# Kernel tuning notes

Hardware: AMD Instinct MI355X
Metric: run time of the kernel (lower is better)

## Reference

```python
import jax, jax.numpy as jnp
import numpy as np

HEADS = 16
ROPE_BASE = 10000.0


def _rope(x):
    # x: [b, h, n, d]. lucidrains partial rotary: RotaryEmbedding(head_dim//2)
    # rotates only the first rot_dim = d//2 channels, interleaved-pair style.
    d = x.shape[-1]
    rot = d // 2
    inv_freq = 1.0 / (ROPE_BASE ** (jnp.arange(0, rot, 2, dtype=jnp.float32) / rot))  # [rot//2]
    pos = jnp.arange(x.shape[2], dtype=jnp.float32)
    freqs = pos[:, None] * inv_freq[None, :]                  # [n, rot//2]
    cos, sin = jnp.cos(freqs), jnp.sin(freqs)
    xr, xp = x[..., :rot], x[..., rot:]
    x1, x2 = xr[..., 0::2], xr[..., 1::2]                     # interleaved pairs
    o1 = x1 * cos - x2 * sin
    o2 = x2 * cos + x1 * sin
    xr_out = jnp.stack([o1, o2], axis=-1).reshape(xr.shape)   # re-interleave
    return jnp.concatenate([xr_out, xp], axis=-1)


def setup_inputs() -> dict:
    key = jax.random.key(0)
    k0, k1 = jax.random.split(key)
    B, N, D = 2, 2048, 2048
    x = jax.random.normal(k0, (B, N, D), dtype=jnp.float32)
    W_qkv = jax.random.normal(k1, (3 * D, D), dtype=jnp.float32) * (D ** -0.5)
    b_qkv = jnp.zeros((3 * D,), dtype=jnp.float32)
    return {"x": x, "W_qkv": W_qkv, "b_qkv": b_qkv}


def reference(x, W_qkv, b_qkv):
    B, N, D = x.shape
    H = HEADS
    hd = D // H
    qkv = x @ W_qkv.T + b_qkv                                  # [b, n, 3d]
    q, k, v = jnp.split(qkv, 3, axis=-1)
    to_heads = lambda t: t.reshape(B, N, H, hd).transpose(0, 2, 1, 3)  # b h n d
    q, k, v = to_heads(q), to_heads(k), to_heads(v)
    q, k = _rope(q), _rope(k)
    scale = 1.0 / np.sqrt(hd)
    scores = jnp.einsum('bhnd,bhmd->bhnm', q, k) * scale
    causal = jnp.tril(jnp.ones((N, N), dtype=bool))
    scores = jnp.where(causal, scores, -jnp.inf)
    attn = jax.nn.softmax(scores, axis=-1)
    y = jnp.einsum('bhnm,bhmd->bhnd', attn, v)
    return y.transpose(0, 2, 1, 3).reshape(B, N, D)
```

## Files before the change

### kernel.cpp

```cpp
#include <hip/hip_runtime.h>
#include <hip/hip_bf16.h>
#include <math.h>

typedef unsigned short u16;
typedef unsigned int u32;
typedef __attribute__((ext_vector_type(8))) short bf16x8;
typedef __attribute__((ext_vector_type(4))) float f32x4;

#define B_ 2
#define N_ 2048
#define D_ 2048
#define H_ 16
#define HD 128
#define GK 2048

__device__ __forceinline__ u16 f2bf(float f) {
  u32 u = __float_as_uint(f);
  u = (u + 0x7fffu + ((u >> 16) & 1u)) >> 16;
  return (u16)u;
}

__device__ __forceinline__ u32 cvtpk(float lo, float hi) {
  u32 r;
  asm("v_cvt_pk_bf16_f32 %0, %1, %2" : "=v"(r) : "v"(lo), "v"(hi));
  return r;
}

__device__ __forceinline__ void gload_lds16(const void* g, void* l) {
  __builtin_amdgcn_global_load_lds(
      (const __attribute__((address_space(1))) u32*)g,
      (__attribute__((address_space(3))) u32*)l, 16, 0, 0);
}

__global__ __launch_bounds__(256) void prep_kernel(
    const float* __restrict__ x, const float* __restrict__ Wq,
    u16* __restrict__ Xb, u16* __restrict__ Wb, float* __restrict__ tbl) {
  const int i0 = blockIdx.x * blockDim.x + threadIdx.x;
  const int st = gridDim.x * blockDim.x;
  const int n4x = (B_ * N_ * D_) / 4;
  const int n4w = (3 * D_ * D_) / 4;
  for (int i = i0; i < n4x + n4w; i += st) {
    float4 v;
    ushort4 o;
    if (i < n4x) {
      v = ((const float4*)x)[i];
      o.x = f2bf(v.x); o.y = f2bf(v.y); o.z = f2bf(v.z); o.w = f2bf(v.w);
      ((ushort4*)Xb)[i] = o;
    } else {
      v = ((const float4*)Wq)[i - n4x];
      o.x = f2bf(v.x); o.y = f2bf(v.y); o.z = f2bf(v.z); o.w = f2bf(v.w);
      ((ushort4*)Wb)[i - n4x] = o;
    }
  }
  for (int i = i0; i < N_ * 32; i += st) {
    int pos = i >> 5, p = i & 31;
    double inv = pow(10000.0, -(double)p / 32.0);
    double a = (double)pos * inv;
    tbl[2 * i]     = (float)cos(a);
    tbl[2 * i + 1] = (float)sin(a);
  }
}

__global__ __launch_bounds__(512, 2) void qkv_gemm_kernel(
    const u16* __restrict__ X, const u16* __restrict__ W,
    const float* __restrict__ bias, const float* __restrict__ tbl,
    u16* __restrict__ Qo, u16* __restrict__ Ko, u16* __restrict__ Vo) {
  __shared__ char smem[147456];
  const int tid = threadIdx.x;
  const int lane = tid & 63;
  const int w = tid >> 6;
  const int wm = w >> 2, wn = w & 3;
  const int l15 = lane & 15, l4 = lane >> 4;

  const int bid = blockIdx.x;
  const int wg = (bid & 7) * 64 + (bid >> 3);
  const int n0 = (wg & 31) * 192;
  const int m0 = (wg >> 5) * 256;

  const int aof0 = (l4 * 16) ^ ((l15 & 7) << 4);
  const int aof1 = (64 + l4 * 16) ^ ((l15 & 7) << 4);
  const int kfA = wm ? aof1 : aof0;
  const int ksA = wm ? aof0 : aof1;

  int srowA[2], scolA[2];
#pragma unroll
  for (int p = 0; p < 2; ++p) {
    int o = (w * 2 + p) * 1024 + lane * 16;
    int lo = o ^ (((o >> 7) & 7) << 4);
    srowA[p] = lo >> 7;
    scolA[p] = (lo & 127) >> 1;
  }
  const int oB = w * 1024 + lane * 16;
  const int loB = oB ^ (((oB >> 7) & 7) << 4);
  const int srowB = loB >> 7, scolB = (loB & 127) >> 1;

  f32x4 acc[8][3];
#pragma unroll
  for (int fm = 0; fm < 8; ++fm)
#pragma unroll
    for (int fn = 0; fn < 3; ++fn)
#pragma unroll
      for (int q = 0; q < 4; ++q) acc[fm][fn][q] = 0.f;

  auto stageA = [&](char* Abase, int half, int k0) {
#pragma unroll
    for (int p = 0; p < 2; ++p) {
      gload_lds16(X + (size_t)(m0 + half * 128 + srowA[p]) * GK + k0 + scolA[p],
                  Abase + half * 16384 + (w * 2 + p) * 1024);
    }
  };
  auto stageB = [&](char* Bbase, int chunk, int k0) {
    gload_lds16(W + (size_t)(n0 + chunk * 64 + srowB) * GK + k0 + scolB,
                Bbase + chunk * 8192 + w * 1024);
  };

  const int NK = GK / 64;

  stageA(smem, 0, 0); stageA(smem, 1, 0);
  stageB(smem + 98304, 0, 0); stageB(smem + 98304, 1, 0); stageB(smem + 98304, 2, 0);
  stageA(smem + 32768, 0, 64); stageA(smem + 32768, 1, 64);
  asm volatile("s_waitcnt vmcnt(4)" ::: "memory");
  __builtin_amdgcn_s_barrier();

  int at = 0;
  for (int T = 0; T < NK; ++T) {
    const int bt = T & 1;
    int an2 = at + 2; if (an2 >= 3) an2 -= 3;
    const char* Ab = smem + at * 32768 + wm * 16384;
    const char* Bb = smem + 98304 + bt * 24576;
    char* Bn = smem + 98304 + (bt ^ 1) * 24576;
    char* An = smem + an2 * 32768;
    const int kn1 = (T + 1) * 64, kn2 = (T + 2) * 64;
    const bool hasB = (T + 1 < NK), hasA = (T + 2 < NK);

    bf16x8 bf_[3], bs_[3], aq[4];

#pragma unroll
    for (int fn = 0; fn < 3; ++fn)
      bf_[fn] = *(const bf16x8*)(Bb + (wn * 48 + fn * 16 + l15) * 128 + kfA);
#pragma unroll
    for (int fm = 0; fm < 4; ++fm)
      aq[fm] = *(const bf16x8*)(Ab + (fm * 16 + l15) * 128 + kfA);
    if (hasB) { stageB(Bn, 0, kn1); stageB(Bn, 1, kn1); stageB(Bn, 2, kn1); }
    __builtin_amdgcn_s_setprio(1);
#pragma unroll
    for (int fm = 0; fm < 4; ++fm)
#pragma unroll
      for (int fn = 0; fn < 3; ++fn)
        acc[fm][fn] = __builtin_amdgcn_mfma_f32_16x16x32_bf16(aq[fm], bf_[fn], acc[fm][fn], 0, 0, 0);
    __builtin_amdgcn_s_setprio(0);

#pragma unroll
    for (int fm = 0; fm < 4; ++fm)
      aq[fm] = *(const bf16x8*)(Ab + ((fm + 4) * 16 + l15) * 128 + kfA);
    __builtin_amdgcn_s_setprio(1);
#pragma unroll
    for (int fm = 0; fm < 4; ++fm)
#pragma unroll
      for (int fn = 0; fn < 3; ++fn)
        acc[fm + 4][fn] = __builtin_amdgcn_mfma_f32_16x16x32_bf16(aq[fm], bf_[fn], acc[fm + 4][fn], 0, 0, 0);
    __builtin_amdgcn_s_setprio(0);

#pragma unroll
    for (int fn = 0; fn < 3; ++fn)
      bs_[fn] = *(const bf16x8*)(Bb + (wn * 48 + fn * 16 + l15) * 128 + ksA);
#pragma unroll
    for (int fm = 0; fm < 4; ++fm)
      aq[fm] = *(const bf16x8*)(Ab + (fm * 16 + l15) * 128 + ksA);
    if (hasA) { stageA(An, 0, kn2); stageA(An, 1, kn2); }
    __builtin_amdgcn_s_setprio(1);
#pragma unroll
    for (int fm = 0; fm < 4; ++fm)
#pragma unroll
      for (int fn = 0; fn < 3; ++fn)
        acc[fm][fn] = __builtin_amdgcn_mfma_f32_16x16x32_bf16(aq[fm], bs_[fn], acc[fm][fn], 0, 0, 0);
    __builtin_amdgcn_s_setprio(0);

#pragma unroll
    for (int fm = 0; fm < 4; ++fm)
      aq[fm] = *(const bf16x8*)(Ab + ((fm + 4) * 16 + l15) * 128 + ksA);
    if (hasA) {
      asm volatile("s_waitcnt vmcnt(4)" ::: "memory");
    } else {
      asm volatile("s_waitcnt vmcnt(0)" ::: "memory");
    }
    __builtin_amdgcn_s_setprio(1);
#pragma unroll
    for (int fm = 0; fm < 4; ++fm)
#pragma unroll
      for (int fn = 0; fn < 3; ++fn)
        acc[fm + 4][fn] = __builtin_amdgcn_mfma_f32_16x16x32_bf16(aq[fm], bs_[fn], acc[fm + 4][fn], 0, 0, 0);
    __builtin_amdgcn_s_setprio(0);
    __builtin_amdgcn_s_barrier();

    at = (at + 1 == 3) ? 0 : at + 1;
  }

  const float QSCALE = 0.08838834764831845f;
#pragma unroll
  for (int fn = 0; fn < 3; ++fn) {
    int gn = n0 + wn * 48 + fn * 16 + l15;
    float bv = bias[gn];
    int sec = gn >> 11;
    int wi = gn & 2047;
    int h = wi >> 7;
    int d = wi & 127;
    u16* dstbase = (sec == 0) ? Qo : (sec == 1) ? Ko : Vo;
    float mulf = (sec == 0) ? QSCALE : 1.f;
    bool doRope = (sec < 2) && (d < 64);
    int pidx = d >> 1;
    bool odd = (d & 1) != 0;
#pragma unroll
    for (int fm = 0; fm < 8; ++fm) {
#pragma unroll
      for (int j = 0; j < 4; ++j) {
        int gm = m0 + wm * 128 + fm * 16 + l4 * 4 + j;
        int bb = gm >> 11;
        int pos = gm & 2047;
        float v = acc[fm][fn][j] + bv;
        float pr = __shfl_xor(v, 1);
        float ov = v;
        if (doRope) {
          float2 cs = ((const float2*)tbl)[pos * 32 + pidx];
          ov = odd ? (v * cs.x + pr * cs.y) : (v * cs.x - pr * cs.y);
        }
        dstbase[(size_t)((bb * H_ + h) * N_ + pos) * HD + d] = f2bf(ov * mulf);
      }
    }
  }
}

__global__ __launch_bounds__(256, 2) void flash_kernel(
    const u16* __restrict__ Q, const u16* __restrict__ K, const u16* __restrict__ V,
    float* __restrict__ Out) {
  __shared__ char smem[51200];

  const int tid = threadIdx.x, lane = tid & 63, w = tid >> 6;
  const int l15 = lane & 15, l4 = lane >> 4;

  const int bid = blockIdx.x;
  const int xcd = bid & 7, s_ = bid >> 3;
  const int bh = xcd * 4 + (s_ & 3);
  const int x = 31 - (s_ >> 2);
  const int bb = bh >> 4, h = bh & 15;
  const size_t base = (size_t)bh * (N_ * HD);
  const int q0 = x * 64;
  const int nt = x + 1;

  bf16x8 qf[4];
  {
    const u16* qp = Q + base + (size_t)(q0 + w * 16 + l15) * HD + l4 * 8;
#pragma unroll
    for (int kf = 0; kf < 4; ++kf) qf[kf] = *(const bf16x8*)(qp + kf * 32);
  }

  float m_r = -1e30f, l_r = 0.f;
  f32x4 accO[8];
#pragma unroll
  for (int df = 0; df < 8; ++df)
#pragma unroll
    for (int q = 0; q < 4; ++q) accO[df][q] = 0.f;

  auto stageK = [&](int buf, int t0) {
    const u16* kb = K + base + (size_t)t0 * HD;
    char* kt = smem + buf * 16384;
#pragma unroll
    for (int i = 0; i < 4; ++i) {
      int c = w * 4 + i;
      int o = c * 1024 + lane * 16;
      int lo = o ^ (((o >> 8) & 7) << 4);
      gload_lds16(kb + (lo >> 1), kt + c * 1024);
    }
  };
  auto loadV = [&](int t0, bf16x8* vr) {
    const u16* vp = V + base + (size_t)(t0 + lane) * HD + w * 32;
#pragma unroll
    for (int i = 0; i < 4; ++i) vr[i] = *(const bf16x8*)(vp + i * 8);
  };
  auto writeV = [&](const bf16x8* vr) {
    u16* vt = (u16*)(smem + 32768);
#pragma unroll
    for (int i = 0; i < 4; ++i)
#pragma unroll
      for (int jj = 0; jj < 8; ++jj)
        vt[(w * 32 + i * 8 + jj) * 72 + lane] = (u16)vr[i][jj];
  };

  const int src0 = l15 + 32 * (l4 & 1);
  const int src1 = src0 + 16;
  const int half = l4 >> 1;
  union U8 { u32 u[4]; bf16x8 v; };

  bf16x8 vreg[4];
  stageK(0, 0);
  loadV(0, vreg);
  __syncthreads();
  writeV(vreg);
  __syncthreads();

  for (int t = 0; t < nt; ++t) {
    const int cur = t & 1;
    const int t0 = t * 64;
    const bool pre = (t + 1 < nt);
    if (pre) { stageK(cur ^ 1, t0 + 64); loadV(t0 + 64, vreg); }

    const char* kt = smem + cur * 16384;
    const u16* vt = (const u16*)(smem + 32768);

    f32x4 s[4];
#pragma unroll
    for (int cf = 0; cf < 4; ++cf) {
#pragma unroll
      for (int q = 0; q < 4; ++q) s[cf][q] = 0.f;
      int row = cf * 16 + l15;
      int sw = (row & 7) << 4;
#pragma unroll
      for (int kf = 0; kf < 4; ++kf) {
        int off = (row * 256 + kf * 64 + l4 * 16) ^ sw;
        bf16x8 kfrag = *(const bf16x8*)(kt + off);
        s[cf] = __builtin_amdgcn_mfma_f32_16x16x32_bf16(kfrag, qf[kf], s[cf], 0, 0, 0);
      }
    }

    const int qbase = q0 + w * 16;
    if (t0 + 63 > qbase) {
      const int qg = qbase + l15;
#pragma unroll
      for (int cf = 0; cf < 4; ++cf)
#pragma unroll
        for (int j = 0; j < 4; ++j) {
          int kvg = t0 + cf * 16 + l4 * 4 + j;
          if (kvg > qg) s[cf][j] = -1e30f;
        }
    }

    float pmax = s[0][0];
#pragma unroll
    for (int cf = 0; cf < 4; ++cf)
#pragma unroll
      for (int j = 0; j < 4; ++j) pmax = fmaxf(pmax, s[cf][j]);
    pmax = fmaxf(pmax, __shfl_xor(pmax, 16));
    pmax = fmaxf(pmax, __shfl_xor(pmax, 32));

    if (!__all(pmax <= m_r + 8.f)) {
      float mn = fmaxf(m_r, pmax);
      float rs = __expf(m_r - mn);
      m_r = mn;
      l_r *= rs;
#pragma unroll
      for (int df = 0; df < 8; ++df)
#pragma unroll
        for (int j = 0; j < 4; ++j) accO[df][j] *= rs;
    }

    u32 pk[4][2];
    float ps = 0.f;
#pragma unroll
    for (int cf = 0; cf < 4; ++cf) {
      float p0 = __expf(s[cf][0] - m_r);
      float p1 = __expf(s[cf][1] - m_r);
      float p2 = __expf(s[cf][2] - m_r);
      float p3 = __expf(s[cf][3] - m_r);
      ps += (p0 + p1) + (p2 + p3);
      pk[cf][0] = cvtpk(p0, p1);
      pk[cf][1] = cvtpk(p2, p3);
    }
    ps += __shfl_xor(ps, 16);
    ps += __shfl_xor(ps, 32);
    l_r += ps;

#pragma unroll
    for (int c = 0; c < 2; ++c) {
      const int c2 = 2 * c;
      u32 a0 = (u32)__shfl((int)pk[c2][0], src0);
      u32 b0 = (u32)__shfl((int)pk[c2 + 1][0], src0);
      u32 a1 = (u32)__shfl((int)pk[c2][1], src0);
      u32 b1 = (u32)__shfl((int)pk[c2 + 1][1], src0);
      u32 a2 = (u32)__shfl((int)pk[c2][0], src1);
      u32 b2 = (u32)__shfl((int)pk[c2 + 1][0], src1);
      u32 a3 = (u32)__shfl((int)pk[c2][1], src1);
      u32 b3 = (u32)__shfl((int)pk[c2 + 1][1], src1);
      U8 pu;
      pu.u[0] = half ? b0 : a0;
      pu.u[1] = half ? b1 : a1;
      pu.u[2] = half ? b2 : a2;
      pu.u[3] = half ? b3 : a3;
#pragma unroll
      for (int df = 0; df < 8; ++df) {
        bf16x8 vf = *(const bf16x8*)(vt + (df * 16 + l15) * 72 + c * 32 + l4 * 8);
        accO[df] = __builtin_amdgcn_mfma_f32_16x16x32_bf16(vf, pu.v, accO[df], 0, 0, 0);
      }
    }

    __syncthreads();
    if (pre) writeV(vreg);
    __syncthreads();
  }

  float* Obuf = (float*)(smem + w * 8448);
  const int l31 = lane & 31;
  {
    float inv = 1.f / l_r;
#pragma unroll
    for (int df = 0; df < 8; ++df) {
      f32x4 v = accO[df];
#pragma unroll
      for (int j = 0; j < 4; ++j) v[j] *= inv;
      *(f32x4*)&Obuf[l15 * 132 + df * 16 + l4 * 4] = v;
    }
  }
#pragma unroll
  for (int p = 0; p < 8; ++p) {
    int row = p * 2 + (lane >> 5);
    f32x4 v = *(const f32x4*)&Obuf[row * 132 + l31 * 4];
    int qg = q0 + w * 16 + row;
    *(f32x4*)&Out[(size_t)(bb * N_ + qg) * D_ + h * HD + l31 * 4] = v;
  }
}

extern "C" void kernel_launch(void* const* d_in, const int* in_sizes, int n_in,
                              void* d_out, int out_size, void* d_ws, size_t ws_size,
                              hipStream_t stream) {
  const float* x  = (const float*)d_in[0];
  const float* Wq = (const float*)d_in[1];
  const float* bq = (const float*)d_in[2];
  float* out = (float*)d_out;
  char* ws = (char*)d_ws;

  u16* Qb  = (u16*)(ws);
  u16* Kb  = (u16*)(ws + 16777216);
  u16* Vb  = (u16*)(ws + 2 * 16777216);
  u16* Xb  = (u16*)(ws + 3 * 16777216);
  u16* Wb  = (u16*)(ws + 4 * 16777216);
  float* tbl = (float*)(ws + 4 * 16777216 + 25165824);

  prep_kernel<<<2048, 256, 0, stream>>>(x, Wq, Xb, Wb, tbl);
  qkv_gemm_kernel<<<512, 512, 0, stream>>>(Xb, Wb, bq, tbl, Qb, Kb, Vb);
  flash_kernel<<<1024, 256, 0, stream>>>(Qb, Kb, Vb, out);
}
```

Baseline: 232.4 us.

## Shrink QKV GEMM tile to 128x192 with 4 waves and double-buffered pipeline

The QKV projection GEMM moves from 512-thread blocks computing 256x192 tiles with triple-buffered A and staggered prefetch to 256-thread blocks computing 128x192 tiles with plain double buffering. Block count doubles to 1024 and the block-to-tile swizzle changes. Shared memory per block drops from 144KB to 80KB, which allows more blocks per CU and spreads the work more evenly across CUs. In exchange each block reuses its data less (more global/L2 traffic per FLOP), and the loop now waits for all outstanding loads (vmcnt(0)) each iteration, which shortens how far loads can run ahead of compute.

```diff
diff --git a/kernel.cpp b/kernel.cpp
--- a/kernel.cpp
+++ b/kernel.cpp
@@ -61,38 +61,32 @@
   }
 }
 
-__global__ __launch_bounds__(512, 2) void qkv_gemm_kernel(
+__global__ __launch_bounds__(256, 2) void qkv_gemm_kernel(
     const u16* __restrict__ X, const u16* __restrict__ W,
     const float* __restrict__ bias, const float* __restrict__ tbl,
     u16* __restrict__ Qo, u16* __restrict__ Ko, u16* __restrict__ Vo) {
-  __shared__ char smem[147456];
+  __shared__ char smem[81920];
   const int tid = threadIdx.x;
   const int lane = tid & 63;
   const int w = tid >> 6;
-  const int wm = w >> 2, wn = w & 3;
   const int l15 = lane & 15, l4 = lane >> 4;
 
   const int bid = blockIdx.x;
-  const int wg = (bid & 7) * 64 + (bid >> 3);
-  const int n0 = (wg & 31) * 192;
-  const int m0 = (wg >> 5) * 256;
+  const int i_ = bid >> 3;
+  const int m0 = (i_ >> 2) * 128;
+  const int n0 = ((bid & 7) * 4 + (i_ & 3)) * 192;
 
   const int aof0 = (l4 * 16) ^ ((l15 & 7) << 4);
   const int aof1 = (64 + l4 * 16) ^ ((l15 & 7) << 4);
-  const int kfA = wm ? aof1 : aof0;
-  const int ksA = wm ? aof0 : aof1;
-
-  int srowA[2], scolA[2];
-#pragma unroll
-  for (int p = 0; p < 2; ++p) {
-    int o = (w * 2 + p) * 1024 + lane * 16;
+
+  int soRow[6], soCol[6];
+#pragma unroll
+  for (int c = 0; c < 6; ++c) {
+    int o = c * 4096 + tid * 16;
     int lo = o ^ (((o >> 7) & 7) << 4);
-    srowA[p] = lo >> 7;
-    scolA[p] = (lo & 127) >> 1;
-  }
-  const int oB = w * 1024 + lane * 16;
-  const int loB = oB ^ (((oB >> 7) & 7) << 4);
-  const int srowB = loB >> 7, scolB = (loB & 127) >> 1;
+    soRow[c] = lo >> 7;
+    soCol[c] = (lo & 127) >> 1;
+  }
 
   f32x4 acc[8][3];
 #pragma unroll
@@ -102,104 +96,96 @@
 #pragma unroll
       for (int q = 0; q < 4; ++q) acc[fm][fn][q] = 0.f;
 
-  auto stageA = [&](char* Abase, int half, int k0) {
-#pragma unroll
-    for (int p = 0; p < 2; ++p) {
-      gload_lds16(X + (size_t)(m0 + half * 128 + srowA[p]) * GK + k0 + scolA[p],
-                  Abase + half * 16384 + (w * 2 + p) * 1024);
-    }
+  auto stageA = [&](char* Ab, int k0) {
+#pragma unroll
+    for (int c = 0; c < 4; ++c)
+      gload_lds16(X + (size_t)(m0 + soRow[c]) * GK + k0 + soCol[c],
+                  Ab + c * 4096 + tid * 16);
   };
-  auto stageB = [&](char* Bbase, int chunk, int k0) {
-    gload_lds16(W + (size_t)(n0 + chunk * 64 + srowB) * GK + k0 + scolB,
-                Bbase + chunk * 8192 + w * 1024);
+  auto stageB = [&](char* Bb, int k0) {
+#pragma unroll
+    for (int c = 0; c < 6; ++c)
+      gload_lds16(W + (size_t)(n0 + soRow[c]) * GK + k0 + soCol[c],
+                  Bb + c * 4096 + tid * 16);
   };
 
   const int NK = GK / 64;
 
-  stageA(smem, 0, 0); stageA(smem, 1, 0);
-  stageB(smem + 98304, 0, 0); stageB(smem + 98304, 1, 0); stageB(smem + 98304, 2, 0);
-  stageA(smem + 32768, 0, 64); stageA(smem + 32768, 1, 64);
-  asm volatile("s_waitcnt vmcnt(4)" ::: "memory");
+  stageA(smem, 0);
+  stageB(smem + 32768, 0);
+  asm volatile("s_waitcnt vmcnt(0)" ::: "memory");
   __builtin_amdgcn_s_barrier();
 
-  int at = 0;
   for (int T = 0; T < NK; ++T) {
-    const int bt = T & 1;
-    int an2 = at + 2; if (an2 >= 3) an2 -= 3;
-    const char* Ab = smem + at * 32768 + wm * 16384;
-    const char* Bb = smem + 98304 + bt * 24576;
-    char* Bn = smem + 98304 + (bt ^ 1) * 24576;
-    char* An = smem + an2 * 32768;
-    const int kn1 = (T + 1) * 64, kn2 = (T + 2) * 64;
-    const bool hasB = (T + 1 < NK), hasA = (T + 2 < NK);
-
-    bf16x8 bf_[3], bs_[3], aq[4];
+    const int cb = T & 1;
+    const char* Ab = smem + cb * 16384;
+    const char* Bb = smem + 32768 + cb * 24576;
+    char* An = smem + (cb ^ 1) * 16384;
+    char* Bn = smem + 32768 + (cb ^ 1) * 24576;
+    const int kn = (T + 1) * 64;
+    const bool nx = (T + 1 < NK);
+
+    bf16x8 bl[3], bh[3], aq[4];
 
 #pragma unroll
     for (int fn = 0; fn < 3; ++fn)
-      bf_[fn] = *(const bf16x8*)(Bb + (wn * 48 + fn * 16 + l15) * 128 + kfA);
-#pragma unroll
-    for (int fm = 0; fm < 4; ++fm)
-      aq[fm] = *(const bf16x8*)(Ab + (fm * 16 + l15) * 128 + kfA);
-    if (hasB) { stageB(Bn, 0, kn1); stageB(Bn, 1, kn1); stageB(Bn, 2, kn1); }
+      bl[fn] = *(const bf16x8*)(Bb + (w * 48 + fn * 16 + l15) * 128 + aof0);
+#pragma unroll
+    for (int fm = 0; fm < 4; ++fm)
+      aq[fm] = *(const bf16x8*)(Ab + (fm * 16 + l15) * 128 + aof0);
+    if (nx) stageB(Bn, kn);
     __builtin_amdgcn_s_setprio(1);
 #pragma unroll
     for (int fm = 0; fm < 4; ++fm)
 #pragma unroll
       for (int fn = 0; fn < 3; ++fn)
-        acc[fm][fn] = __builtin_amdgcn_mfma_f32_16x16x32_bf16(aq[fm], bf_[fn], acc[fm][fn], 0, 0, 0);
+        acc[fm][fn] = __builtin_amdgcn_mfma_f32_16x16x32_bf16(aq[fm], bl[fn], acc[fm][fn], 0, 0, 0);
     __builtin_amdgcn_s_setprio(0);
 
 #pragma unroll
     for (int fm = 0; fm < 4; ++fm)
-      aq[fm] = *(const bf16x8*)(Ab + ((fm + 4) * 16 + l15) * 128 + kfA);
+      aq[fm] = *(const bf16x8*)(Ab + ((fm + 4) * 16 + l15) * 128 + aof0);
     __builtin_amdgcn_s_setprio(1);
 #pragma unroll
     for (int fm = 0; fm < 4; ++fm)
 #pragma unroll
       for (int fn = 0; fn < 3; ++fn)
-        acc[fm + 4][fn] = __builtin_amdgcn_mfma_f32_16x16x32_bf16(aq[fm], bf_[fn], acc[fm + 4][fn], 0, 0, 0);
+        acc[fm + 4][fn] = __builtin_amdgcn_mfma_f32_16x16x32_bf16(aq[fm], bl[fn], acc[fm + 4][fn], 0, 0, 0);
     __builtin_amdgcn_s_setprio(0);
 
 #pragma unroll
     for (int fn = 0; fn < 3; ++fn)
-      bs_[fn] = *(const bf16x8*)(Bb + (wn * 48 + fn * 16 + l15) * 128 + ksA);
-#pragma unroll
-    for (int fm = 0; fm < 4; ++fm)
-      aq[fm] = *(const bf16x8*)(Ab + (fm * 16 + l15) * 128 + ksA);
-    if (hasA) { stageA(An, 0, kn2); stageA(An, 1, kn2); }
+      bh[fn] = *(const bf16x8*)(Bb + (w * 48 + fn * 16 + l15) * 128 + aof1);
+#pragma unroll
+    for (int fm = 0; fm < 4; ++fm)
+      aq[fm] = *(const bf16x8*)(Ab + (fm * 16 + l15) * 128 + aof1);
+    if (nx) stageA(An, kn);
     __builtin_amdgcn_s_setprio(1);
 #pragma unroll
     for (int fm = 0; fm < 4; ++fm)
 #pragma unroll
       for (int fn = 0; fn < 3; ++fn)
-        acc[fm][fn] = __builtin_amdgcn_mfma_f32_16x16x32_bf16(aq[fm], bs_[fn], acc[fm][fn], 0, 0, 0);
+        acc[fm][fn] = __builtin_amdgcn_mfma_f32_16x16x32_bf16(aq[fm], bh[fn], acc[fm][fn], 0, 0, 0);
     __builtin_amdgcn_s_setprio(0);
 
 #pragma unroll
     for (int fm = 0; fm < 4; ++fm)
-      aq[fm] = *(const bf16x8*)(Ab + ((fm + 4) * 16 + l15) * 128 + ksA);
-    if (hasA) {
-      asm volatile("s_waitcnt vmcnt(4)" ::: "memory");
-    } else {
-      asm volatile("s_waitcnt vmcnt(0)" ::: "memory");
-    }
+      aq[fm] = *(const bf16x8*)(Ab + ((fm + 4) * 16 + l15) * 128 + aof1);
+    asm volatile("s_waitcnt vmcnt(0)" ::: "memory");
     __builtin_amdgcn_s_setprio(1);
 #pragma unroll
     for (int fm = 0; fm < 4; ++fm)
 #pragma unroll
       for (int fn = 0; fn < 3; ++fn)
-        acc[fm + 4][fn] = __builtin_amdgcn_mfma_f32_16x16x32_bf16(aq[fm], bs_[fn], acc[fm + 4][fn], 0, 0, 0);
+        acc[fm + 4][fn] = __builtin_amdgcn_mfma_f32_16x16x32_bf16(aq[fm], bh[fn], acc[fm + 4][fn], 0, 0, 0);
     __builtin_amdgcn_s_setprio(0);
     __builtin_amdgcn_s_barrier();
-
-    at = (at + 1 == 3) ? 0 : at + 1;
   }
 
   const float QSCALE = 0.08838834764831845f;
 #pragma unroll
   for (int fn = 0; fn < 3; ++fn) {
-    int gn = n0 + wn * 48 + fn * 16 + l15;
+    int gn = n0 + w * 48 + fn * 16 + l15;
     float bv = bias[gn];
     int sec = gn >> 11;
     int wi = gn & 2047;
@@ -214,7 +200,7 @@
     for (int fm = 0; fm < 8; ++fm) {
 #pragma unroll
       for (int j = 0; j < 4; ++j) {
-        int gm = m0 + wm * 128 + fm * 16 + l4 * 4 + j;
+        int gm = m0 + fm * 16 + l4 * 4 + j;
         int bb = gm >> 11;
         int pos = gm & 2047;
         float v = acc[fm][fn][j] + bv;
@@ -435,6 +421,6 @@
   float* tbl = (float*)(ws + 4 * 16777216 + 25165824);
 
   prep_kernel<<<2048, 256, 0, stream>>>(x, Wq, Xb, Wb, tbl);
-  qkv_gemm_kernel<<<512, 512, 0, stream>>>(Xb, Wb, bq, tbl, Qb, Kb, Vb);
+  qkv_gemm_kernel<<<1024, 256, 0, stream>>>(Xb, Wb, bq, tbl, Qb, Kb, Vb);
   flash_kernel<<<1024, 256, 0, stream>>>(Qb, Kb, Vb, out);
 }
```

New measurement: 236.6 us. About the same (+1.8%).
